# Kernel optimization log

Measured on AMD Instinct MI355X. Metric: run time of the kernel, lower is better.

## Reference

```python
import jax, jax.numpy as jnp
import numpy as np

N = 50000   # num_nodes
R = 8       # num_relations
H = 128     # hidden_l
L = 32      # num_labels
E = 1600000 # num_edges


def setup_inputs() -> dict:
    key = jax.random.key(0)
    ks = jax.random.split(key, 8)
    edge_index = jax.random.randint(ks[0], (2, E), 0, N, dtype=jnp.int64)
    edge_type = jax.random.randint(ks[1], (E,), 0, R, dtype=jnp.int64)
    # layer 1: in_channels = num_nodes (x=None -> one-hot features)
    weight1 = jax.random.normal(ks[2], (R, N, H), dtype=jnp.float32) * 0.02
    root1 = jax.random.normal(ks[3], (N, H), dtype=jnp.float32) * 0.02
    bias1 = jnp.zeros((H,), dtype=jnp.float32)
    # layer 2: hidden -> labels
    weight2 = jax.random.normal(ks[4], (R, H, L), dtype=jnp.float32) * 0.05
    root2 = jax.random.normal(ks[5], (H, L), dtype=jnp.float32) * 0.05
    bias2 = jnp.zeros((L,), dtype=jnp.float32)
    return {"weight1": weight1, "root1": root1, "bias1": bias1,
            "weight2": weight2, "root2": root2, "bias2": bias2,
            "edge_index": edge_index, "edge_type": edge_type}


def _rel_mean_agg(msg, dst, et, num_nodes, num_rel):
    """PyG RGCNConv aggr='mean': mean over incoming edges per (node, relation),
    then sum over relations. msg: [E, F]."""
    seg = dst * num_rel + et  # combined (node, relation) segment id
    sums = jax.ops.segment_sum(msg, seg, num_segments=num_nodes * num_rel)
    cnt = jax.ops.segment_sum(jnp.ones((msg.shape[0],), msg.dtype), seg,
                              num_segments=num_nodes * num_rel)
    mean = sums / jnp.maximum(cnt, 1.0)[:, None]  # zero where count==0
    return mean.reshape(num_nodes, num_rel, -1).sum(axis=1)  # [N, F]


def reference(weight1, root1, bias1, weight2, root2, bias2, edge_index, edge_type):
    src, dst = edge_index[0], edge_index[1]
    # ---- layer 1 (x=None): message = weight1[r, src] row gather ----
    msg1 = weight1[edge_type, src]                      # [E, H]
    x = _rel_mean_agg(msg1, dst, edge_type, N, R) + root1 + bias1
    x = jax.nn.relu(x)
    # ---- layer 2: per-relation matmul then gather ----
    xw = jnp.einsum('nh,rhl->nrl', x, weight2)          # [N, R, L]
    msg2 = xw[src, edge_type]                           # [E, L]
    out = _rel_mean_agg(msg2, dst, edge_type, N, R) + x @ root2 + bias2
    return jax.nn.sigmoid(out)
```

## Files before the change

kernel.cpp:

```cpp
#include <hip/hip_runtime.h>
#include <math.h>

#define NN 50000
#define RR 8
#define HH 128
#define LL 32
#define EE 1600000
#define BW 128
#define NB 391
#define PB 782

#define FMA4(A, V, C) { A.x += (V).x*(C); A.y += (V).y*(C); A.z += (V).z*(C); A.w += (V).w*(C); }

typedef __attribute__((ext_vector_type(8))) short short8_t;
typedef __attribute__((ext_vector_type(4))) float f32x4_t;

__device__ __forceinline__ float bflo(unsigned u) { return __uint_as_float(u << 16); }
__device__ __forceinline__ float bfhi(unsigned u) { return __uint_as_float(u & 0xFFFF0000u); }
__device__ __forceinline__ unsigned bfpk(float a, float b) {
    unsigned ua = __float_as_uint(a), ub = __float_as_uint(b);
    ua = (ua + 0x7FFFu + ((ua >> 16) & 1u)) >> 16;
    ub = (ub + 0x7FFFu + ((ub >> 16) & 1u)) >> 16;
    return ua | (ub << 16);
}
__device__ __forceinline__ unsigned short bf16r(float f) {
    unsigned u = __float_as_uint(f);
    return (unsigned short)((u + 0x7FFFu + ((u >> 16) & 1u)) >> 16);
}

__global__ __launch_bounds__(256) void conv_hist(const float4* __restrict__ w1,
                                                 const float* __restrict__ w2,
                                                 const int* __restrict__ ei,
                                                 uint4* __restrict__ w1b,
                                                 unsigned* __restrict__ wtb,
                                                 unsigned* __restrict__ ph) {
    __shared__ unsigned h[NB];
    int b = blockIdx.x, tid = threadIdx.x;
    if (b < 25000) {
        size_t t = (size_t)b * 256 + tid;
        float4 a = w1[2 * t], c = w1[2 * t + 1];
        uint4 o;
        o.x = bfpk(a.x, a.y); o.y = bfpk(a.z, a.w);
        o.z = bfpk(c.x, c.y); o.w = bfpk(c.z, c.w);
        w1b[t] = o;
    } else if (b == 25000) {
        int c = tid, r = c >> 5, l = c & 31;
        const float* wp = w2 + (size_t)r * HH * LL + l;
        for (int k = 0; k < HH; k += 2)
            wtb[c * 64 + (k >> 1)] = bfpk(wp[k * LL], wp[(k + 1) * LL]);
    } else {
        int blk = b - 25001;
        for (int i = tid; i < NB; i += 256) h[i] = 0;
        __syncthreads();
        int base = blk * 2048;
#pragma unroll
        for (int k = 0; k < 8; ++k) {
            int e = base + k * 256 + tid;
            if (e < EE) atomicAdd(&h[(unsigned)ei[EE + e] >> 7], 1u);
        }
        __syncthreads();
        for (int i = tid; i < NB; i += 256) ph[blk * NB + i] = h[i];
    }
}

__global__ __launch_bounds__(512) void bscan_kernel(const unsigned* __restrict__ ph,
                                                    unsigned* __restrict__ boff,
                                                    unsigned* __restrict__ bcur,
                                                    unsigned* __restrict__ node_off,
                                                    unsigned* __restrict__ srcr) {
    __shared__ unsigned s[512];
    int t = threadIdx.x;
    unsigned v = 0;
    if (t < NB)
        for (int blk = 0; blk < PB; ++blk) v += ph[blk * NB + t];
    s[t] = v; __syncthreads();
    for (int off = 1; off < 512; off <<= 1) {
        unsigned u = (t >= off) ? s[t - off] : 0; __syncthreads();
        if (t >= off) s[t] += u; __syncthreads();
    }
    if (t < NB) { unsigned o = s[t] - v; boff[t] = o; bcur[t] = o; }
    if (t == 0) { boff[NB] = EE; node_off[NN] = EE; }
    if (t < 16) srcr[EE + t] = 0;
}

__global__ __launch_bounds__(256) void part_kernel(const int* __restrict__ ei,
                                                   const int* __restrict__ et,
                                                   unsigned* __restrict__ bcur,
                                                   unsigned* __restrict__ tmp) {
    __shared__ unsigned h[NB];
    for (int i = threadIdx.x; i < NB; i += 256) h[i] = 0;
    __syncthreads();
    int base = blockIdx.x * 2048;
    unsigned pay[8]; int bk[8];
#pragma unroll
    for (int k = 0; k < 8; ++k) {
        int e = base + k * 256 + threadIdx.x;
        bk[k] = -1;
        if (e < EE) {
            unsigned sN = (unsigned)ei[e], d = (unsigned)ei[EE + e], r = (unsigned)et[e];
            bk[k] = (int)(d >> 7);
            pay[k] = sN | (r << 16) | ((d & 127u) << 19);
            atomicAdd(&h[bk[k]], 1u);
        }
    }
    __syncthreads();
    for (int i = threadIdx.x; i < NB; i += 256) {
        unsigned c = h[i];
        h[i] = c ? atomicAdd(&bcur[i], c) : 0u;
    }
    __syncthreads();
#pragma unroll
    for (int k = 0; k < 8; ++k)
        if (bk[k] >= 0) {
            unsigned p = atomicAdd(&h[bk[k]], 1u);
            tmp[p] = pay[k];
        }
}

__global__ __launch_bounds__(256) void finalize_kernel(const unsigned* __restrict__ boff,
                                                       const unsigned* __restrict__ tmp,
                                                       unsigned* __restrict__ node_off,
                                                       float* __restrict__ inv,
                                                       unsigned* __restrict__ srcr) {
    __shared__ unsigned cnt[BW * RR];
    __shared__ unsigned cur[BW];
    __shared__ unsigned excl[BW];
    int b = blockIdx.x, t = threadIdx.x;
    unsigned lo = boff[b], hi = boff[b + 1];
    int nn0 = b * BW;
    int nloc = NN - nn0 < BW ? NN - nn0 : BW;
    for (int i = t; i < BW * RR; i += 256) cnt[i] = 0;
    __syncthreads();
    for (unsigned i = lo + t; i < hi; i += 256) {
        unsigned v = tmp[i];
        atomicAdd(&cnt[((v >> 19) & 127u) * RR + ((v >> 16) & 7u)], 1u);
    }
    __syncthreads();
    unsigned own = 0;
    if (t < BW) {
#pragma unroll
        for (int r = 0; r < RR; ++r) own += cnt[t * RR + r];
        excl[t] = own;
    }
    __syncthreads();
    for (int off = 1; off < BW; off <<= 1) {
        unsigned u = 0;
        if (t < BW && t >= off) u = excl[t - off];
        __syncthreads();
        if (t < BW && t >= off) excl[t] += u;
        __syncthreads();
    }
    if (t < nloc) {
        unsigned o = lo + excl[t] - own;
        node_off[nn0 + t] = o;
        cur[t] = o;
    }
    __syncthreads();
    for (int i = t; i < nloc * RR; i += 256) {
        unsigned c = cnt[i];
        inv[(size_t)nn0 * RR + i] = c ? 1.f / (float)c : 0.f;
    }
    for (unsigned i = lo + t; i < hi; i += 256) {
        unsigned v = tmp[i];
        unsigned p = atomicAdd(&cur[(v >> 19) & 127u], 1u);
        srcr[p] = v & 0x7FFFFu;
    }
}

__global__ __launch_bounds__(256) void l1_gather(const unsigned* __restrict__ node_off,
                                                 const unsigned* __restrict__ srcr,
                                                 const float* __restrict__ inv,
                                                 const uint4* __restrict__ w1b,
                                                 const float* __restrict__ root1,
                                                 const float* __restrict__ bias1,
                                                 uint4* __restrict__ xb) {
    int wid = threadIdx.x >> 6, lane = threadIdx.x & 63;
    int n = blockIdx.x * 4 + wid;
    if (n >= NN) return;
    int q = lane >> 4, ql = lane & 15;
    int beg = node_off[n], end = node_off[n + 1];
    int cnt = end - beg;
    int nfull = cnt >> 4;
    float myinv = inv[n * RR + (lane & 7)];
    float4 a0 = {0.f, 0.f, 0.f, 0.f}, a1 = {0.f, 0.f, 0.f, 0.f};
    int e = beg + q;
#define GATH(K, C) {                                                        \
        unsigned ss = (K) & 0xFFFFu, rr = (K) >> 16;                        \
        uint4 v = w1b[((size_t)rr * NN + ss) * 16 + ql];                    \
        a0.x = fmaf(bflo(v.x), (C), a0.x); a0.y = fmaf(bfhi(v.x), (C), a0.y); \
        a0.z = fmaf(bflo(v.y), (C), a0.z); a0.w = fmaf(bfhi(v.y), (C), a0.w); \
        a1.x = fmaf(bflo(v.z), (C), a1.x); a1.y = fmaf(bfhi(v.z), (C), a1.y); \
        a1.z = fmaf(bflo(v.w), (C), a1.z); a1.w = fmaf(bfhi(v.w), (C), a1.w); }
#pragma unroll 1
    for (int it = 0; it < nfull; ++it, e += 16) {
        unsigned k0 = srcr[e], k1 = srcr[e + 4], k2 = srcr[e + 8], k3 = srcr[e + 12];
        float c0 = __shfl(myinv, (int)(k0 >> 16));
        float c1 = __shfl(myinv, (int)(k1 >> 16));
        float c2 = __shfl(myinv, (int)(k2 >> 16));
        float c3 = __shfl(myinv, (int)(k3 >> 16));
        GATH(k0, c0); GATH(k1, c1); GATH(k2, c2); GATH(k3, c3);
    }
    {
        unsigned k0 = srcr[e], k1 = srcr[e + 4], k2 = srcr[e + 8], k3 = srcr[e + 12];
        float c0 = __shfl(myinv, (int)(k0 >> 16));
        float c1 = __shfl(myinv, (int)(k1 >> 16));
        float c2 = __shfl(myinv, (int)(k2 >> 16));
        float c3 = __shfl(myinv, (int)(k3 >> 16));
        if (e < end)      GATH(k0, c0);
        if (e + 4 < end)  GATH(k1, c1);
        if (e + 8 < end)  GATH(k2, c2);
        if (e + 12 < end) GATH(k3, c3);
    }
#undef GATH
#define RED(c) { c += __shfl_xor(c, 16); c += __shfl_xor(c, 32); }
    RED(a0.x); RED(a0.y); RED(a0.z); RED(a0.w);
    RED(a1.x); RED(a1.y); RED(a1.z); RED(a1.w);
#undef RED
    if (q == 0) {
        const float4* rt = (const float4*)(root1 + (size_t)n * HH);
        const float4* bs = (const float4*)bias1;
        float4 rA = rt[2 * ql], rB = rt[2 * ql + 1];
        float4 bA = bs[2 * ql], bB = bs[2 * ql + 1];
        float o0 = fmaxf(a0.x + rA.x + bA.x, 0.f);
        float o1 = fmaxf(a0.y + rA.y + bA.y, 0.f);
        float o2 = fmaxf(a0.z + rA.z + bA.z, 0.f);
        float o3 = fmaxf(a0.w + rA.w + bA.w, 0.f);
        float o4 = fmaxf(a1.x + rB.x + bB.x, 0.f);
        float o5 = fmaxf(a1.y + rB.y + bB.y, 0.f);
        float o6 = fmaxf(a1.z + rB.z + bB.z, 0.f);
        float o7 = fmaxf(a1.w + rB.w + bB.w, 0.f);
        uint4 o;
        o.x = bfpk(o0, o1); o.y = bfpk(o2, o3);
        o.z = bfpk(o4, o5); o.w = bfpk(o6, o7);
        xb[(size_t)n * 16 + ql] = o;
    }
}

__global__ __launch_bounds__(256) void xw_mfma(const unsigned* __restrict__ xb,
                                               const unsigned* __restrict__ wtb,
                                               unsigned short* __restrict__ xwb) {
    int tid = threadIdx.x, wid = tid >> 6, l = tid & 63;
    int bn = blockIdx.x >> 2;
    int bc = blockIdx.x & 3;
    int col = bc * 64 + wid * 16 + (l & 15);
    int kq = l >> 4;
    short8_t bfr[4];
    const unsigned* wcol = wtb + col * 64;
#pragma unroll
    for (int ks = 0; ks < 4; ++ks)
        bfr[ks] = *reinterpret_cast<const short8_t*>(wcol + ks * 16 + kq * 4);
    int n0 = bn * 64;
#pragma unroll
    for (int sub = 0; sub < 4; ++sub) {
        int row = n0 + sub * 16 + (l & 15);
        int rc = row < NN ? row : NN - 1;
        const unsigned* xr = xb + (size_t)rc * 64;
        f32x4_t acc = {0.f, 0.f, 0.f, 0.f};
#pragma unroll
        for (int ks = 0; ks < 4; ++ks) {
            short8_t a = *reinterpret_cast<const short8_t*>(xr + ks * 16 + kq * 4);
            acc = __builtin_amdgcn_mfma_f32_16x16x32_bf16(a, bfr[ks], acc, 0, 0, 0);
        }
        int orow0 = n0 + sub * 16 + kq * 4;
#pragma unroll
        for (int j = 0; j < 4; ++j) {
            int orow = orow0 + j;
            if (orow < NN) xwb[(size_t)orow * 256 + col] = bf16r(acc[j]);
        }
    }
}

__global__ __launch_bounds__(256) void l2_gather(const unsigned* __restrict__ node_off,
                                                 const unsigned* __restrict__ srcr,
                                                 const float* __restrict__ inv,
                                                 const uint2* __restrict__ xwb,
                                                 const unsigned* __restrict__ xb,
                                                 const float* __restrict__ root2,
                                                 const float* __restrict__ bias2,
                                                 float* __restrict__ out) {
    int wid = threadIdx.x >> 6, lane = threadIdx.x & 63;
    int n = blockIdx.x * 4 + wid;
    if (n >= NN) return;
    int g = lane >> 3, gl = lane & 7;
    int beg = node_off[n], end = node_off[n + 1];
    int cnt = end - beg;
    int nfull = cnt >> 4;
    float myinv = inv[n * RR + (lane & 7)];
    float4 acc = {0.f, 0.f, 0.f, 0.f};
    int e = beg + g;
#define GATH2(K, C) {                                              \
        unsigned ss = (K) & 0xFFFFu, rr = (K) >> 16;               \
        uint2 v = xwb[((size_t)ss * RR + rr) * 8 + gl];            \
        acc.x = fmaf(bflo(v.x), (C), acc.x);                       \
        acc.y = fmaf(bfhi(v.x), (C), acc.y);                       \
        acc.z = fmaf(bflo(v.y), (C), acc.z);                       \
        acc.w = fmaf(bfhi(v.y), (C), acc.w); }
#pragma unroll 1
    for (int it = 0; it < nfull; ++it, e += 16) {
        unsigned k0 = srcr[e], k1 = srcr[e + 8];
        float c0 = __shfl(myinv, (int)(k0 >> 16));
        float c1 = __shfl(myinv, (int)(k1 >> 16));
        GATH2(k0, c0);
        GATH2(k1, c1);
    }
    {
        unsigned k0 = srcr[e], k1 = srcr[e + 8];
        float c0 = __shfl(myinv, (int)(k0 >> 16));
        float c1 = __shfl(myinv, (int)(k1 >> 16));
        if (e < end)     GATH2(k0, c0);
        if (e + 8 < end) GATH2(k1, c1);
    }
#undef GATH2
    {
        const uint4* xr = (const uint4*)(xb + (size_t)n * 64);
        uint4 u0 = xr[g * 2], u1 = xr[g * 2 + 1];
        float xv[16] = {bflo(u0.x), bfhi(u0.x), bflo(u0.y), bfhi(u0.y),
                        bflo(u0.z), bfhi(u0.z), bflo(u0.w), bfhi(u0.w),
                        bflo(u1.x), bfhi(u1.x), bflo(u1.y), bfhi(u1.y),
                        bflo(u1.z), bfhi(u1.z), bflo(u1.w), bfhi(u1.w)};
        const float4* rp = (const float4*)root2 + g * 16 * 8 + gl;
#pragma unroll
        for (int i = 0; i < 16; ++i) {
            float4 w = rp[i * 8];
            FMA4(acc, w, xv[i]);
        }
    }
#define RED3(c) { c += __shfl_xor(c, 8); c += __shfl_xor(c, 16); c += __shfl_xor(c, 32); }
    RED3(acc.x); RED3(acc.y); RED3(acc.z); RED3(acc.w);
#undef RED3
    if (lane < 8) {
        float4 b = ((const float4*)bias2)[gl];
        float4 z;
        z.x = 1.f / (1.f + expf(-(acc.x + b.x)));
        z.y = 1.f / (1.f + expf(-(acc.y + b.y)));
        z.z = 1.f / (1.f + expf(-(acc.z + b.z)));
        z.w = 1.f / (1.f + expf(-(acc.w + b.w)));
        ((float4*)(out + (size_t)n * LL))[gl] = z;
    }
}

extern "C" void kernel_launch(void* const* d_in, const int* in_sizes, int n_in,
                              void* d_out, int out_size, void* d_ws, size_t ws_size,
                              hipStream_t stream) {
    const float* w1    = (const float*)d_in[0];
    const float* root1 = (const float*)d_in[1];
    const float* bias1 = (const float*)d_in[2];
    const float* w2    = (const float*)d_in[3];
    const float* root2 = (const float*)d_in[4];
    const float* bias2 = (const float*)d_in[5];
    const int*   ei    = (const int*)d_in[6];
    const int*   et    = (const int*)d_in[7];
    float* out = (float*)d_out;

    float*    inv      = (float*)d_ws;
    unsigned* node_off = (unsigned*)(inv + 400000);
    unsigned* boff     = node_off + 50004;
    unsigned* bcur     = boff + 400;
    unsigned* ph       = bcur + 400;
    unsigned* srcr     = ph + 305768;
    unsigned* xb       = srcr + 1600020;
    unsigned* wtb      = xb + 3200000;
    unsigned* w1b      = wtb + 16384;
    unsigned* xwb      = w1b + 25600000;
    unsigned* tmp      = xwb;

    conv_hist<<<25000 + 1 + PB, 256, 0, stream>>>((const float4*)w1, w2, ei,
                                                  (uint4*)w1b, wtb, ph);
    bscan_kernel<<<1, 512, 0, stream>>>(ph, boff, bcur, node_off, srcr);
    part_kernel<<<PB, 256, 0, stream>>>(ei, et, bcur, tmp);
    finalize_kernel<<<NB, 256, 0, stream>>>(boff, tmp, node_off, inv, srcr);
    l1_gather<<<(NN + 3) / 4, 256, 0, stream>>>(node_off, srcr, inv, (const uint4*)w1b,
                                                root1, bias1, (uint4*)xb);
    xw_mfma<<<((NN + 63) / 64) * 4, 256, 0, stream>>>(xb, wtb, (unsigned short*)xwb);
    l2_gather<<<(NN + 3) / 4, 256, 0, stream>>>(node_off, srcr, inv, (const uint2*)xwb,
                                                xb, root2, bias2, out);
}
```

Baseline: 319.1 us.

## Parallelize bucket reduction, fuse weight conversion with partition, prefetch edge keys

The per-bucket count reduction that one 512-thread block did serially over 782 partial histograms now runs in its own kernel with one block per bucket and wavefront shuffles. The bf16 weight conversion moves out of the histogram kernel and into the partition kernel's launch, so the partition runs alongside the large conversion rather than after it. Both gather loops now software-prefetch the next iteration's edge keys. The cost is one extra kernel launch and a few more registers in the gather kernels.

```diff
diff --git a/kernel.cpp b/kernel.cpp
--- a/kernel.cpp
+++ b/kernel.cpp
@@ -28,51 +28,43 @@
     return (unsigned short)((u + 0x7FFFu + ((u >> 16) & 1u)) >> 16);
 }
 
-__global__ __launch_bounds__(256) void conv_hist(const float4* __restrict__ w1,
-                                                 const float* __restrict__ w2,
-                                                 const int* __restrict__ ei,
-                                                 uint4* __restrict__ w1b,
-                                                 unsigned* __restrict__ wtb,
-                                                 unsigned* __restrict__ ph) {
+__global__ __launch_bounds__(256) void hist_kernel(const int* __restrict__ ei,
+                                                   unsigned* __restrict__ ph) {
     __shared__ unsigned h[NB];
-    int b = blockIdx.x, tid = threadIdx.x;
-    if (b < 25000) {
-        size_t t = (size_t)b * 256 + tid;
-        float4 a = w1[2 * t], c = w1[2 * t + 1];
-        uint4 o;
-        o.x = bfpk(a.x, a.y); o.y = bfpk(a.z, a.w);
-        o.z = bfpk(c.x, c.y); o.w = bfpk(c.z, c.w);
-        w1b[t] = o;
-    } else if (b == 25000) {
-        int c = tid, r = c >> 5, l = c & 31;
-        const float* wp = w2 + (size_t)r * HH * LL + l;
-        for (int k = 0; k < HH; k += 2)
-            wtb[c * 64 + (k >> 1)] = bfpk(wp[k * LL], wp[(k + 1) * LL]);
-    } else {
-        int blk = b - 25001;
-        for (int i = tid; i < NB; i += 256) h[i] = 0;
-        __syncthreads();
-        int base = blk * 2048;
-#pragma unroll
-        for (int k = 0; k < 8; ++k) {
-            int e = base + k * 256 + tid;
-            if (e < EE) atomicAdd(&h[(unsigned)ei[EE + e] >> 7], 1u);
-        }
-        __syncthreads();
-        for (int i = tid; i < NB; i += 256) ph[blk * NB + i] = h[i];
-    }
-}
-
-__global__ __launch_bounds__(512) void bscan_kernel(const unsigned* __restrict__ ph,
+    int blk = blockIdx.x, tid = threadIdx.x;
+    for (int i = tid; i < NB; i += 256) h[i] = 0;
+    __syncthreads();
+    int base = blk * 2048;
+#pragma unroll
+    for (int k = 0; k < 8; ++k) {
+        int e = base + k * 256 + tid;
+        if (e < EE) atomicAdd(&h[(unsigned)ei[EE + e] >> 7], 1u);
+    }
+    __syncthreads();
+    for (int i = tid; i < NB; i += 256) ph[blk * NB + i] = h[i];
+}
+
+__global__ __launch_bounds__(256) void bred_kernel(const unsigned* __restrict__ ph,
+                                                   unsigned* __restrict__ bcnt) {
+    __shared__ unsigned s[4];
+    int b = blockIdx.x, t = threadIdx.x;
+    unsigned v = 0;
+    for (int j = t; j < PB; j += 256) v += ph[j * NB + b];
+    v += __shfl_down(v, 32); v += __shfl_down(v, 16); v += __shfl_down(v, 8);
+    v += __shfl_down(v, 4);  v += __shfl_down(v, 2);  v += __shfl_down(v, 1);
+    if ((t & 63) == 0) s[t >> 6] = v;
+    __syncthreads();
+    if (t == 0) bcnt[b] = s[0] + s[1] + s[2] + s[3];
+}
+
+__global__ __launch_bounds__(512) void bscan_kernel(const unsigned* __restrict__ bcnt,
                                                     unsigned* __restrict__ boff,
                                                     unsigned* __restrict__ bcur,
                                                     unsigned* __restrict__ node_off,
                                                     unsigned* __restrict__ srcr) {
     __shared__ unsigned s[512];
     int t = threadIdx.x;
-    unsigned v = 0;
-    if (t < NB)
-        for (int blk = 0; blk < PB; ++blk) v += ph[blk * NB + t];
+    unsigned v = (t < NB) ? bcnt[t] : 0;
     s[t] = v; __syncthreads();
     for (int off = 1; off < 512; off <<= 1) {
         unsigned u = (t >= off) ? s[t - off] : 0; __syncthreads();
@@ -83,18 +75,39 @@
     if (t < 16) srcr[EE + t] = 0;
 }
 
-__global__ __launch_bounds__(256) void part_kernel(const int* __restrict__ ei,
-                                                   const int* __restrict__ et,
-                                                   unsigned* __restrict__ bcur,
-                                                   unsigned* __restrict__ tmp) {
+__global__ __launch_bounds__(256) void part_conv(const int* __restrict__ ei,
+                                                 const int* __restrict__ et,
+                                                 unsigned* __restrict__ bcur,
+                                                 unsigned* __restrict__ tmp,
+                                                 const float4* __restrict__ w1,
+                                                 const float* __restrict__ w2,
+                                                 uint4* __restrict__ w1b,
+                                                 unsigned* __restrict__ wtb) {
     __shared__ unsigned h[NB];
-    for (int i = threadIdx.x; i < NB; i += 256) h[i] = 0;
-    __syncthreads();
-    int base = blockIdx.x * 2048;
+    int b = blockIdx.x, tid = threadIdx.x;
+    if (b >= PB) {
+        if (b < PB + 25000) {
+            size_t t = (size_t)(b - PB) * 256 + tid;
+            float4 a = w1[2 * t], c = w1[2 * t + 1];
+            uint4 o;
+            o.x = bfpk(a.x, a.y); o.y = bfpk(a.z, a.w);
+            o.z = bfpk(c.x, c.y); o.w = bfpk(c.z, c.w);
+            w1b[t] = o;
+        } else {
+            int c = tid, r = c >> 5, l = c & 31;
+            const float* wp = w2 + (size_t)r * HH * LL + l;
+            for (int k = 0; k < HH; k += 2)
+                wtb[c * 64 + (k >> 1)] = bfpk(wp[k * LL], wp[(k + 1) * LL]);
+        }
+        return;
+    }
+    for (int i = tid; i < NB; i += 256) h[i] = 0;
+    __syncthreads();
+    int base = b * 2048;
     unsigned pay[8]; int bk[8];
 #pragma unroll
     for (int k = 0; k < 8; ++k) {
-        int e = base + k * 256 + threadIdx.x;
+        int e = base + k * 256 + tid;
         bk[k] = -1;
         if (e < EE) {
             unsigned sN = (unsigned)ei[e], d = (unsigned)ei[EE + e], r = (unsigned)et[e];
@@ -104,7 +117,7 @@
         }
     }
     __syncthreads();
-    for (int i = threadIdx.x; i < NB; i += 256) {
+    for (int i = tid; i < NB; i += 256) {
         unsigned c = h[i];
         h[i] = c ? atomicAdd(&bcur[i], c) : 0u;
     }
@@ -184,6 +197,7 @@
     float myinv = inv[n * RR + (lane & 7)];
     float4 a0 = {0.f, 0.f, 0.f, 0.f}, a1 = {0.f, 0.f, 0.f, 0.f};
     int e = beg + q;
+    unsigned kp0 = srcr[e], kp1 = srcr[e + 4], kp2 = srcr[e + 8], kp3 = srcr[e + 12];
 #define GATH(K, C) {                                                        \
         unsigned ss = (K) & 0xFFFFu, rr = (K) >> 16;                        \
         uint4 v = w1b[((size_t)rr * NN + ss) * 16 + ql];                    \
@@ -192,8 +206,10 @@
         a1.x = fmaf(bflo(v.z), (C), a1.x); a1.y = fmaf(bfhi(v.z), (C), a1.y); \
         a1.z = fmaf(bflo(v.w), (C), a1.z); a1.w = fmaf(bfhi(v.w), (C), a1.w); }
 #pragma unroll 1
-    for (int it = 0; it < nfull; ++it, e += 16) {
-        unsigned k0 = srcr[e], k1 = srcr[e + 4], k2 = srcr[e + 8], k3 = srcr[e + 12];
+    for (int it = 0; it < nfull; ++it) {
+        unsigned k0 = kp0, k1 = kp1, k2 = kp2, k3 = kp3;
+        e += 16;
+        kp0 = srcr[e]; kp1 = srcr[e + 4]; kp2 = srcr[e + 8]; kp3 = srcr[e + 12];
         float c0 = __shfl(myinv, (int)(k0 >> 16));
         float c1 = __shfl(myinv, (int)(k1 >> 16));
         float c2 = __shfl(myinv, (int)(k2 >> 16));
@@ -201,15 +217,14 @@
         GATH(k0, c0); GATH(k1, c1); GATH(k2, c2); GATH(k3, c3);
     }
     {
-        unsigned k0 = srcr[e], k1 = srcr[e + 4], k2 = srcr[e + 8], k3 = srcr[e + 12];
-        float c0 = __shfl(myinv, (int)(k0 >> 16));
-        float c1 = __shfl(myinv, (int)(k1 >> 16));
-        float c2 = __shfl(myinv, (int)(k2 >> 16));
-        float c3 = __shfl(myinv, (int)(k3 >> 16));
-        if (e < end)      GATH(k0, c0);
-        if (e + 4 < end)  GATH(k1, c1);
-        if (e + 8 < end)  GATH(k2, c2);
-        if (e + 12 < end) GATH(k3, c3);
+        float c0 = __shfl(myinv, (int)(kp0 >> 16));
+        float c1 = __shfl(myinv, (int)(kp1 >> 16));
+        float c2 = __shfl(myinv, (int)(kp2 >> 16));
+        float c3 = __shfl(myinv, (int)(kp3 >> 16));
+        if (e < end)      GATH(kp0, c0);
+        if (e + 4 < end)  GATH(kp1, c1);
+        if (e + 8 < end)  GATH(kp2, c2);
+        if (e + 12 < end) GATH(kp3, c3);
     }
 #undef GATH
 #define RED(c) { c += __shfl_xor(c, 16); c += __shfl_xor(c, 32); }
@@ -288,6 +303,7 @@
     float myinv = inv[n * RR + (lane & 7)];
     float4 acc = {0.f, 0.f, 0.f, 0.f};
     int e = beg + g;
+    unsigned kp0 = srcr[e], kp1 = srcr[e + 8];
 #define GATH2(K, C) {                                              \
         unsigned ss = (K) & 0xFFFFu, rr = (K) >> 16;               \
         uint2 v = xwb[((size_t)ss * RR + rr) * 8 + gl];            \
@@ -296,19 +312,20 @@
         acc.z = fmaf(bflo(v.y), (C), acc.z);                       \
         acc.w = fmaf(bfhi(v.y), (C), acc.w); }
 #pragma unroll 1
-    for (int it = 0; it < nfull; ++it, e += 16) {
-        unsigned k0 = srcr[e], k1 = srcr[e + 8];
+    for (int it = 0; it < nfull; ++it) {
+        unsigned k0 = kp0, k1 = kp1;
+        e += 16;
+        kp0 = srcr[e]; kp1 = srcr[e + 8];
         float c0 = __shfl(myinv, (int)(k0 >> 16));
         float c1 = __shfl(myinv, (int)(k1 >> 16));
         GATH2(k0, c0);
         GATH2(k1, c1);
     }
     {
-        unsigned k0 = srcr[e], k1 = srcr[e + 8];
-        float c0 = __shfl(myinv, (int)(k0 >> 16));
-        float c1 = __shfl(myinv, (int)(k1 >> 16));
-        if (e < end)     GATH2(k0, c0);
-        if (e + 8 < end) GATH2(k1, c1);
+        float c0 = __shfl(myinv, (int)(kp0 >> 16));
+        float c1 = __shfl(myinv, (int)(kp1 >> 16));
+        if (e < end)     GATH2(kp0, c0);
+        if (e + 8 < end) GATH2(kp1, c1);
     }
 #undef GATH2
     {
@@ -356,7 +373,8 @@
     unsigned* node_off = (unsigned*)(inv + 400000);
     unsigned* boff     = node_off + 50004;
     unsigned* bcur     = boff + 400;
-    unsigned* ph       = bcur + 400;
+    unsigned* bcnt     = bcur + 400;
+    unsigned* ph       = bcnt + 400;
     unsigned* srcr     = ph + 305768;
     unsigned* xb       = srcr + 1600020;
     unsigned* wtb      = xb + 3200000;
@@ -364,10 +382,11 @@
     unsigned* xwb      = w1b + 25600000;
     unsigned* tmp      = xwb;
 
-    conv_hist<<<25000 + 1 + PB, 256, 0, stream>>>((const float4*)w1, w2, ei,
-                                                  (uint4*)w1b, wtb, ph);
-    bscan_kernel<<<1, 512, 0, stream>>>(ph, boff, bcur, node_off, srcr);
-    part_kernel<<<PB, 256, 0, stream>>>(ei, et, bcur, tmp);
+    hist_kernel<<<PB, 256, 0, stream>>>(ei, ph);
+    bred_kernel<<<NB, 256, 0, stream>>>(ph, bcnt);
+    bscan_kernel<<<1, 512, 0, stream>>>(bcnt, boff, bcur, node_off, srcr);
+    part_conv<<<PB + 25001, 256, 0, stream>>>(ei, et, bcur, tmp,
+                                              (const float4*)w1, w2, (uint4*)w1b, wtb);
     finalize_kernel<<<NB, 256, 0, stream>>>(boff, tmp, node_off, inv, srcr);
     l1_gather<<<(NN + 3) / 4, 256, 0, stream>>>(node_off, srcr, inv, (const uint4*)w1b,
                                                 root1, bias1, (uint4*)xb);
```

After: 264.3 us (median of 2 runs). -17.2%, faster.
